# Performance work log

Measured on AMD Instinct MI355X. Metric: run time of the kernel, lower is better.

The kernel has to match this reference:

```python
import jax, jax.numpy as jnp
import numpy as np

D_MODEL = 4
FFN_HIDDEN = 8


def setup_inputs() -> dict:
    key = jax.random.key(0)
    ks = jax.random.split(key, 14)
    B, S = 1024, 256
    d, h = D_MODEL, FFN_HIDDEN
    sc = 0.5  # small init scale
    return {
        "x": jax.random.normal(ks[0], (B, S), dtype=jnp.float32),
        # torch nn.Linear weights are [out_features, in_features]
        "emb_w": jax.random.normal(ks[1], (d, 1), dtype=jnp.float32) * sc,
        "emb_b": jax.random.normal(ks[2], (d,), dtype=jnp.float32) * sc,
        "q_w": jax.random.normal(ks[3], (d, d), dtype=jnp.float32) * sc,
        "q_b": jax.random.normal(ks[4], (d,), dtype=jnp.float32) * sc,
        "k_w": jax.random.normal(ks[5], (d, d), dtype=jnp.float32) * sc,
        "k_b": jax.random.normal(ks[6], (d,), dtype=jnp.float32) * sc,
        "v_w": jax.random.normal(ks[7], (d, d), dtype=jnp.float32) * sc,
        "v_b": jax.random.normal(ks[8], (d,), dtype=jnp.float32) * sc,
        "f1_w": jax.random.normal(ks[9], (h, d), dtype=jnp.float32) * sc,
        "f1_b": jax.random.normal(ks[10], (h,), dtype=jnp.float32) * sc,
        "f2_w": jax.random.normal(ks[11], (1, h), dtype=jnp.float32) * sc,
        "f2_b": jax.random.normal(ks[12], (1,), dtype=jnp.float32) * sc,
    }


def reference(x, emb_w, emb_b, q_w, q_b, k_w, k_b, v_w, v_b, f1_w, f1_b, f2_w, f2_b):
    d = emb_w.shape[0]
    # x: [B,S] -> unsqueeze(-1) -> Linear(1,d): [B,S,d]
    h = x[..., None] * emb_w[:, 0] + emb_b  # broadcast [B,S,1]*[d] -> [B,S,d]
    q = jnp.einsum('bsd,ed->bse', h, q_w) + q_b
    k = jnp.einsum('bsd,ed->bse', h, k_w) + k_b
    v = jnp.einsum('bsd,ed->bse', h, v_w) + v_b
    scores = jnp.einsum('bqd,bkd->bqk', q, k) / jnp.sqrt(jnp.float32(d))
    probs = jax.nn.softmax(scores, axis=-1)
    out = jnp.einsum('bqk,bkd->bqd', probs, v)  # [B,S,d]
    pooled = out.mean(axis=1)  # [B,d]
    hid = jax.nn.relu(pooled @ f1_w.T + f1_b)  # [B,8]
    return hid @ f2_w.T + f2_b  # [B,1]
```

## Files before the change

### kernel.cpp

```cpp
#include <hip/hip_runtime.h>

#define SEQ 256
#define ROWS 2
#define KCH 32
#define NTHREADS 1024
#define LOG2E 1.44269504088896340736f

__global__ __launch_bounds__(NTHREADS, 8) void pico_transformer_kernel(
    const float* __restrict__ x,
    const float* __restrict__ emb_w,
    const float* __restrict__ emb_b,
    const float* __restrict__ q_w,
    const float* __restrict__ q_b,
    const float* __restrict__ k_w,
    const float* __restrict__ k_b,
    const float* __restrict__ v_w,
    const float* __restrict__ v_b,
    const float* __restrict__ f1_w,
    const float* __restrict__ f1_b,
    const float* __restrict__ f2_w,
    const float* __restrict__ f2_b,
    float* __restrict__ out)
{
    __shared__ float xs[ROWS][SEQ];
    __shared__ float cons[27];
    __shared__ float red_mx[8], red_mn[8];
    __shared__ float gnode[ROWS][KCH];
    __shared__ float coef[ROWS][KCH];
    __shared__ float mids[ROWS], radinvs[ROWS];
    __shared__ float red_sum[8];

    const int tid = threadIdx.x;
    const int blk = blockIdx.x;

    if (tid < ROWS * SEQ) {
        const int r   = tid >> 8;
        const int col = tid & 255;
        float xv = x[(blk * ROWS + r) * SEQ + col];
        xs[r][col] = xv;
        float mx = xv, mn = xv;
        #pragma unroll
        for (int off = 32; off > 0; off >>= 1) {
            mx = fmaxf(mx, __shfl_down(mx, off, 64));
            mn = fminf(mn, __shfl_down(mn, off, 64));
        }
        if ((tid & 63) == 0) { red_mx[tid >> 6] = mx; red_mn[tid >> 6] = mn; }
    }

    if (tid == 0) {
        float we[4], be[4], Aq[4], Bq[4], Ak[4], Av[4], Bv[4];
        #pragma unroll
        for (int d = 0; d < 4; ++d) { we[d] = emb_w[d]; be[d] = emb_b[d]; }
        #pragma unroll
        for (int e = 0; e < 4; ++e) {
            float aq = 0.f, bq = 0.f, ak = 0.f, av = 0.f, bv = 0.f;
            #pragma unroll
            for (int d = 0; d < 4; ++d) {
                aq += q_w[e*4+d] * we[d];
                bq += q_w[e*4+d] * be[d];
                ak += k_w[e*4+d] * we[d];
                av += v_w[e*4+d] * we[d];
                bv += v_w[e*4+d] * be[d];
            }
            Aq[e] = aq; Bq[e] = bq + q_b[e]; Ak[e] = ak;
            Av[e] = av; Bv[e] = bv + v_b[e];
        }
        float c1 = 0.f, c3 = 0.f;
        #pragma unroll
        for (int d = 0; d < 4; ++d) { c1 += Aq[d]*Ak[d]; c3 += Bq[d]*Ak[d]; }
        cons[0] = 0.5f * c1 * LOG2E;
        cons[1] = 0.5f * c3 * LOG2E;
        #pragma unroll
        for (int j = 0; j < 8; ++j) {
            float u = 0.f, w = 0.f;
            #pragma unroll
            for (int d = 0; d < 4; ++d) {
                u += f1_w[j*4+d] * Av[d];
                w += f1_w[j*4+d] * Bv[d];
            }
            cons[2 + j]  = u;
            cons[10 + j] = w + f1_b[j];
            cons[18 + j] = f2_w[j];
        }
        cons[26] = f2_b[0];
    }

    __syncthreads();

    {
        const int r = tid >> 9;
        const int i = (tid >> 4) & 31;
        const int s = tid & 15;

        const int rb = r << 2;
        const float XMAX = fmaxf(fmaxf(red_mx[rb], red_mx[rb+1]), fmaxf(red_mx[rb+2], red_mx[rb+3]));
        const float XMIN = fminf(fminf(red_mn[rb], red_mn[rb+1]), fminf(red_mn[rb+2], red_mn[rb+3]));

        const float c0  = cons[0], c1v = cons[1];
        const float mid = fmaf(c0, 0.5f * (XMAX + XMIN), c1v);
        const float rad = fabsf(c0) * 0.5f * (XMAX - XMIN);

        const float tau_i = cospif((float)(2 * i + 1) * (1.0f / 64.0f));
        const float t     = fmaf(rad, tau_i, mid);
        const float m2    = (t >= 0.f) ? t * XMAX : t * XMIN;
        const float nm2   = -m2;

        float num = 0.f, den = 0.f;
        #pragma unroll
        for (int j = 0; j < 16; ++j) {
            float xk = xs[r][s + 16 * j];
            float e  = __builtin_amdgcn_exp2f(fmaf(t, xk, nm2));
            num = fmaf(xk, e, num);
            den += e;
        }
        #pragma unroll
        for (int off = 8; off > 0; off >>= 1) {
            num += __shfl_xor(num, off, 64);
            den += __shfl_xor(den, off, 64);
        }
        if (s == 0) gnode[r][i] = num / den;
    }
    __syncthreads();

    if (tid < 2 * KCH) {
        const int r = tid >> 5;
        const int m = tid & 31;
        float acc = 0.f;
        #pragma unroll
        for (int i = 0; i < KCH; ++i) {
            float Tmi = cospif((float)(m * (2 * i + 1)) * (1.0f / 64.0f));
            acc = fmaf(gnode[r][i], Tmi, acc);
        }
        coef[r][m] = acc * ((m == 0) ? (1.0f / KCH) : (2.0f / KCH));
        if (m == 0) {
            const int rb = r << 2;
            const float XMAX = fmaxf(fmaxf(red_mx[rb], red_mx[rb+1]), fmaxf(red_mx[rb+2], red_mx[rb+3]));
            const float XMIN = fminf(fminf(red_mn[rb], red_mn[rb+1]), fminf(red_mn[rb+2], red_mn[rb+3]));
            const float c0 = cons[0];
            mids[r]    = fmaf(c0, 0.5f * (XMAX + XMIN), cons[1]);
            float rad  = fabsf(c0) * 0.5f * (XMAX - XMIN);
            radinvs[r] = (rad > 1e-30f) ? (1.0f / rad) : 0.f;
        }
    }
    __syncthreads();

    if (tid < ROWS * SEQ) {
        const int r = tid >> 8;
        const int q = tid & 255;
        const float t   = fmaf(cons[0], xs[r][q], cons[1]);
        const float tau = (t - mids[r]) * radinvs[r];
        const float tt  = 2.f * tau;
        float b1 = 0.f, b2 = 0.f;
        #pragma unroll
        for (int m = KCH - 1; m >= 1; --m) {
            float b0 = fmaf(tt, b1, coef[r][m] - b2);
            b2 = b1; b1 = b0;
        }
        float g = fmaf(tau, b1, coef[r][0] - b2);

        #pragma unroll
        for (int off = 32; off > 0; off >>= 1) g += __shfl_down(g, off, 64);
        if ((tid & 63) == 0) red_sum[tid >> 6] = g;
    }
    __syncthreads();

    if (tid < ROWS) {
        const int rb = tid << 2;
        float G = (red_sum[rb] + red_sum[rb+1] + red_sum[rb+2] + red_sum[rb+3]) * (1.0f / SEQ);
        float acc = cons[26];
        #pragma unroll
        for (int j = 0; j < 8; ++j) {
            float hv = fmaxf(G * cons[2 + j] + cons[10 + j], 0.f);
            acc += hv * cons[18 + j];
        }
        out[blk * ROWS + tid] = acc;
    }
}

extern "C" void kernel_launch(void* const* d_in, const int* in_sizes, int n_in,
                              void* d_out, int out_size, void* d_ws, size_t ws_size,
                              hipStream_t stream) {
    const float* x     = (const float*)d_in[0];
    const float* emb_w = (const float*)d_in[1];
    const float* emb_b = (const float*)d_in[2];
    const float* q_w   = (const float*)d_in[3];
    const float* q_b   = (const float*)d_in[4];
    const float* k_w   = (const float*)d_in[5];
    const float* k_b   = (const float*)d_in[6];
    const float* v_w   = (const float*)d_in[7];
    const float* v_b   = (const float*)d_in[8];
    const float* f1_w  = (const float*)d_in[9];
    const float* f1_b  = (const float*)d_in[10];
    const float* f2_w  = (const float*)d_in[11];
    const float* f2_b  = (const float*)d_in[12];
    float* out = (float*)d_out;

    const int B = in_sizes[0] / SEQ;
    pico_transformer_kernel<<<B / ROWS, NTHREADS, 0, stream>>>(
        x, emb_w, emb_b, q_w, q_b, k_w, k_b, v_w, v_b,
        f1_w, f1_b, f2_w, f2_b, out);
}
```

Baseline: 85.68 us.

## Halve Chebyshev degree and parallelize coefficient transform and constant setup

Reduces the Chebyshev interpolation of the per-query softmax-weighted mean from 32 to 16 nodes, halving node evaluations and shortening the Clenshaw recurrence. The coefficient transform now uses 512 threads with shuffle reductions in place of a serial 32-term loop in 64 threads. The constant precomputation is spread over 8 threads, and mid/radius are recomputed per thread instead of going through shared memory. Lower degree risks accuracy loss on inputs with a wide range.

```diff
diff --git a/kernel.cpp b/kernel.cpp
--- a/kernel.cpp
+++ b/kernel.cpp
@@ -2,7 +2,7 @@
 
 #define SEQ 256
 #define ROWS 2
-#define KCH 32
+#define KCH 16
 #define NTHREADS 1024
 #define LOG2E 1.44269504088896340736f
 
@@ -27,7 +27,6 @@
     __shared__ float red_mx[8], red_mn[8];
     __shared__ float gnode[ROWS][KCH];
     __shared__ float coef[ROWS][KCH];
-    __shared__ float mids[ROWS], radinvs[ROWS];
     __shared__ float red_sum[8];
 
     const int tid = threadIdx.x;
@@ -47,50 +46,58 @@
         if ((tid & 63) == 0) { red_mx[tid >> 6] = mx; red_mn[tid >> 6] = mn; }
     }
 
-    if (tid == 0) {
-        float we[4], be[4], Aq[4], Bq[4], Ak[4], Av[4], Bv[4];
+    if (tid < 8) {
+        const int j = tid;
+        float we[4], be[4], Av[4], Bv[4];
         #pragma unroll
         for (int d = 0; d < 4; ++d) { we[d] = emb_w[d]; be[d] = emb_b[d]; }
         #pragma unroll
         for (int e = 0; e < 4; ++e) {
-            float aq = 0.f, bq = 0.f, ak = 0.f, av = 0.f, bv = 0.f;
+            float av = 0.f, bv = 0.f;
             #pragma unroll
             for (int d = 0; d < 4; ++d) {
-                aq += q_w[e*4+d] * we[d];
-                bq += q_w[e*4+d] * be[d];
-                ak += k_w[e*4+d] * we[d];
                 av += v_w[e*4+d] * we[d];
                 bv += v_w[e*4+d] * be[d];
             }
-            Aq[e] = aq; Bq[e] = bq + q_b[e]; Ak[e] = ak;
             Av[e] = av; Bv[e] = bv + v_b[e];
         }
-        float c1 = 0.f, c3 = 0.f;
-        #pragma unroll
-        for (int d = 0; d < 4; ++d) { c1 += Aq[d]*Ak[d]; c3 += Bq[d]*Ak[d]; }
-        cons[0] = 0.5f * c1 * LOG2E;
-        cons[1] = 0.5f * c3 * LOG2E;
-        #pragma unroll
-        for (int j = 0; j < 8; ++j) {
-            float u = 0.f, w = 0.f;
+        float u = 0.f, w = 0.f;
+        #pragma unroll
+        for (int d = 0; d < 4; ++d) {
+            u += f1_w[j*4+d] * Av[d];
+            w += f1_w[j*4+d] * Bv[d];
+        }
+        cons[2 + j]  = u;
+        cons[10 + j] = w + f1_b[j];
+        cons[18 + j] = f2_w[j];
+        if (j == 0) {
+            float Aq[4], Bq[4], Ak[4];
             #pragma unroll
-            for (int d = 0; d < 4; ++d) {
-                u += f1_w[j*4+d] * Av[d];
-                w += f1_w[j*4+d] * Bv[d];
+            for (int e = 0; e < 4; ++e) {
+                float aq = 0.f, bq = 0.f, ak = 0.f;
+                #pragma unroll
+                for (int d = 0; d < 4; ++d) {
+                    aq += q_w[e*4+d] * we[d];
+                    bq += q_w[e*4+d] * be[d];
+                    ak += k_w[e*4+d] * we[d];
+                }
+                Aq[e] = aq; Bq[e] = bq + q_b[e]; Ak[e] = ak;
             }
-            cons[2 + j]  = u;
-            cons[10 + j] = w + f1_b[j];
-            cons[18 + j] = f2_w[j];
-        }
-        cons[26] = f2_b[0];
+            float c1 = 0.f, c3 = 0.f;
+            #pragma unroll
+            for (int d = 0; d < 4; ++d) { c1 += Aq[d]*Ak[d]; c3 += Bq[d]*Ak[d]; }
+            cons[0]  = 0.5f * c1 * LOG2E;
+            cons[1]  = 0.5f * c3 * LOG2E;
+            cons[26] = f2_b[0];
+        }
     }
 
     __syncthreads();
 
     {
         const int r = tid >> 9;
-        const int i = (tid >> 4) & 31;
-        const int s = tid & 15;
+        const int i = (tid >> 5) & 15;
+        const int s = tid & 31;
 
         const int rb = r << 2;
         const float XMAX = fmaxf(fmaxf(red_mx[rb], red_mx[rb+1]), fmaxf(red_mx[rb+2], red_mx[rb+3]));
@@ -100,21 +107,21 @@
         const float mid = fmaf(c0, 0.5f * (XMAX + XMIN), c1v);
         const float rad = fabsf(c0) * 0.5f * (XMAX - XMIN);
 
-        const float tau_i = cospif((float)(2 * i + 1) * (1.0f / 64.0f));
+        const float tau_i = cospif((float)(2 * i + 1) * (1.0f / 32.0f));
         const float t     = fmaf(rad, tau_i, mid);
         const float m2    = (t >= 0.f) ? t * XMAX : t * XMIN;
         const float nm2   = -m2;
 
         float num = 0.f, den = 0.f;
         #pragma unroll
-        for (int j = 0; j < 16; ++j) {
-            float xk = xs[r][s + 16 * j];
+        for (int j = 0; j < 8; ++j) {
+            float xk = xs[r][s + 32 * j];
             float e  = __builtin_amdgcn_exp2f(fmaf(t, xk, nm2));
             num = fmaf(xk, e, num);
             den += e;
         }
         #pragma unroll
-        for (int off = 8; off > 0; off >>= 1) {
+        for (int off = 16; off > 0; off >>= 1) {
             num += __shfl_xor(num, off, 64);
             den += __shfl_xor(den, off, 64);
         }
@@ -122,33 +129,31 @@
     }
     __syncthreads();
 
-    if (tid < 2 * KCH) {
-        const int r = tid >> 5;
-        const int m = tid & 31;
-        float acc = 0.f;
-        #pragma unroll
-        for (int i = 0; i < KCH; ++i) {
-            float Tmi = cospif((float)(m * (2 * i + 1)) * (1.0f / 64.0f));
-            acc = fmaf(gnode[r][i], Tmi, acc);
-        }
-        coef[r][m] = acc * ((m == 0) ? (1.0f / KCH) : (2.0f / KCH));
-        if (m == 0) {
-            const int rb = r << 2;
-            const float XMAX = fmaxf(fmaxf(red_mx[rb], red_mx[rb+1]), fmaxf(red_mx[rb+2], red_mx[rb+3]));
-            const float XMIN = fminf(fminf(red_mn[rb], red_mn[rb+1]), fminf(red_mn[rb+2], red_mn[rb+3]));
-            const float c0 = cons[0];
-            mids[r]    = fmaf(c0, 0.5f * (XMAX + XMIN), cons[1]);
-            float rad  = fabsf(c0) * 0.5f * (XMAX - XMIN);
-            radinvs[r] = (rad > 1e-30f) ? (1.0f / rad) : 0.f;
-        }
+    if (tid < ROWS * KCH * KCH) {
+        const int r = tid >> 8;
+        const int m = (tid >> 4) & 15;
+        const int i = tid & 15;
+        float Tmi  = cospif((float)(m * (2 * i + 1)) * (1.0f / 32.0f));
+        float prod = gnode[r][i] * Tmi;
+        #pragma unroll
+        for (int off = 8; off > 0; off >>= 1) prod += __shfl_xor(prod, off, 64);
+        if (i == 0) coef[r][m] = prod * ((m == 0) ? (1.0f / KCH) : (2.0f / KCH));
     }
     __syncthreads();
 
     if (tid < ROWS * SEQ) {
         const int r = tid >> 8;
         const int q = tid & 255;
-        const float t   = fmaf(cons[0], xs[r][q], cons[1]);
-        const float tau = (t - mids[r]) * radinvs[r];
+        const int rb = r << 2;
+        const float XMAX = fmaxf(fmaxf(red_mx[rb], red_mx[rb+1]), fmaxf(red_mx[rb+2], red_mx[rb+3]));
+        const float XMIN = fminf(fminf(red_mn[rb], red_mn[rb+1]), fminf(red_mn[rb+2], red_mn[rb+3]));
+        const float c0  = cons[0];
+        const float mid = fmaf(c0, 0.5f * (XMAX + XMIN), cons[1]);
+        const float rad = fabsf(c0) * 0.5f * (XMAX - XMIN);
+        const float radinv = (rad > 1e-30f) ? (1.0f / rad) : 0.f;
+
+        const float t   = fmaf(c0, xs[r][q], cons[1]);
+        const float tau = (t - mid) * radinv;
         const float tt  = 2.f * tau;
         float b1 = 0.f, b2 = 0.f;
         #pragma unroll
```

After: 81.09 us. 1.06x faster.
